# Optimization experiments

Hardware: AMD Instinct MI355X
Metric: run time of the kernel (lower is better)

## Reference

```python
import jax, jax.numpy as jnp
import numpy as np

HEADS = 4
DIM_HEAD = 32
DIM = 128
B, N, Hq, Wg = 2, 6, 32, 32   # batch, cameras, BEV grid
HK, WK = 28, 60               # image feature map


def _ln(x, g, b, eps=1e-5):
    mu = jnp.mean(x, axis=-1, keepdims=True)
    var = jnp.mean((x - mu) ** 2, axis=-1, keepdims=True)
    return (x - mu) * jax.lax.rsqrt(var + eps) * g + b


def setup_inputs() -> dict:
    key = jax.random.key(0)
    ks = jax.random.split(key, 12)
    s = 0.05  # weight scale to keep softmax logits well-conditioned
    inp = {
        'q': jax.random.normal(ks[0], (B, N, DIM, Hq, Wg), jnp.float32),
        'k': jax.random.normal(ks[1], (B, N, DIM, HK, WK), jnp.float32),
        'v': jax.random.normal(ks[2], (B, N, DIM, HK, WK), jnp.float32),
        'skip': jax.random.normal(ks[3], (B, DIM, Hq, Wg), jnp.float32),
        'q_ln_g': jnp.ones((DIM,), jnp.float32),
        'q_ln_b': jnp.zeros((DIM,), jnp.float32),
        'Wq': s * jax.random.normal(ks[4], (DIM, HEADS * DIM_HEAD), jnp.float32),
        'bq': jnp.zeros((HEADS * DIM_HEAD,), jnp.float32),
        'k_ln_g': jnp.ones((DIM,), jnp.float32),
        'k_ln_b': jnp.zeros((DIM,), jnp.float32),
        'Wk': s * jax.random.normal(ks[5], (DIM, HEADS * DIM_HEAD), jnp.float32),
        'bk': jnp.zeros((HEADS * DIM_HEAD,), jnp.float32),
        'v_ln_g': jnp.ones((DIM,), jnp.float32),
        'v_ln_b': jnp.zeros((DIM,), jnp.float32),
        'Wv': s * jax.random.normal(ks[6], (DIM, HEADS * DIM_HEAD), jnp.float32),
        'bv': jnp.zeros((HEADS * DIM_HEAD,), jnp.float32),
        'Wp': s * jax.random.normal(ks[7], (HEADS * DIM_HEAD, DIM), jnp.float32),
        'bp': jnp.zeros((DIM,), jnp.float32),
        'pre_g': jnp.ones((DIM,), jnp.float32),
        'pre_b': jnp.zeros((DIM,), jnp.float32),
        'W1': s * jax.random.normal(ks[8], (DIM, 2 * DIM), jnp.float32),
        'b1': jnp.zeros((2 * DIM,), jnp.float32),
        'W2': s * jax.random.normal(ks[9], (2 * DIM, DIM), jnp.float32),
        'b2': jnp.zeros((DIM,), jnp.float32),
        'post_g': jnp.ones((DIM,), jnp.float32),
        'post_b': jnp.zeros((DIM,), jnp.float32),
    }
    return inp


def reference(q, k, v, skip, q_ln_g, q_ln_b, Wq, bq, k_ln_g, k_ln_b, Wk, bk,
              v_ln_g, v_ln_b, Wv, bv, Wp, bp, pre_g, pre_b,
              W1, b1, W2, b2, post_g, post_b):
    b, n, d, H, W = q.shape
    Q = H * W
    K = k.shape[3] * k.shape[4]
    m, dh = HEADS, DIM_HEAD
    # b n d H W -> b n Q d   /  b n d h w -> b n K d  /  b (n K) d
    qf = q.transpose(0, 1, 3, 4, 2).reshape(b, n, Q, d)
    kf = k.transpose(0, 1, 3, 4, 2).reshape(b, n, K, d)
    vf = v.transpose(0, 1, 3, 4, 2).reshape(b, n * K, d)
    # norm -> linear, then split heads: b ... (m dh) -> (b m) ... dh
    qh = (_ln(qf, q_ln_g, q_ln_b) @ Wq + bq).reshape(b, n, Q, m, dh)
    qh = qh.transpose(0, 3, 1, 2, 4).reshape(b * m, n, Q, dh)
    kh = (_ln(kf, k_ln_g, k_ln_b) @ Wk + bk).reshape(b, n, K, m, dh)
    kh = kh.transpose(0, 3, 1, 2, 4).reshape(b * m, n, K, dh)
    vh = (_ln(vf, v_ln_g, v_ln_b) @ Wv + bv).reshape(b, n * K, m, dh)
    vh = vh.transpose(0, 2, 1, 3).reshape(b * m, n * K, dh)
    scale = dh ** -0.5
    dot = scale * jnp.einsum('anqd,ankd->anqk', qh, kh)   # (b m) n Q K
    dot = dot.transpose(0, 2, 1, 3).reshape(b * m, Q, n * K)  # fold views into keys
    att = jax.nn.softmax(dot, axis=-1)
    a = jnp.einsum('aqk,akd->aqd', att, vh)               # (b m) Q dh
    a = a.reshape(b, m, Q, dh).transpose(0, 2, 1, 3).reshape(b, Q, m * dh)
    z = a @ Wp + bp
    z = z + skip.transpose(0, 2, 3, 1).reshape(b, Q, d)
    z = _ln(z, pre_g, pre_b)
    z = z + (jax.nn.gelu(z @ W1 + b1, approximate=False) @ W2 + b2)
    z = _ln(z, post_g, post_b)
    return z.reshape(b, H, W, d).transpose(0, 3, 1, 2)
```

## Files before the change

### kernel.cpp

```cpp
#include <hip/hip_runtime.h>
#include <math.h>

#define NCAM 6
#define BSZ 2
#define SQL 1024
#define SKL 1680
#define NHEAD 4
#define DHEAD 32
#define QSCALE 0.25503494f

typedef unsigned short ushort_t;
typedef unsigned int uint_t;
typedef __attribute__((ext_vector_type(8))) short short8;
typedef __attribute__((ext_vector_type(4))) float f32x4;

#define MFMA16 __builtin_amdgcn_mfma_f32_16x16x32_bf16

__device__ __forceinline__ ushort_t f2bf(float x) {
  uint_t u = __builtin_bit_cast(uint_t, x);
  u += 0x7FFFu + ((u >> 16) & 1u);
  return (ushort_t)(u >> 16);
}

__device__ __forceinline__ float fast_gelu(float x) {
  const float ax = fabsf(x) * 0.70710678118654752f;
  const float tt = __builtin_amdgcn_rcpf(fmaf(0.3275911f, ax, 1.f));
  float poly = fmaf(tt, 1.061405429f, -1.453152027f);
  poly = fmaf(tt, poly, 1.421413741f);
  poly = fmaf(tt, poly, -0.284496736f);
  poly = fmaf(tt, poly, 0.254829592f);
  poly *= tt;
  const float e = __builtin_amdgcn_exp2f(-ax * ax * 1.4426950408889634f);
  float er = fmaf(-poly, e, 1.f);
  er = copysignf(er, x);
  return 0.5f * x * (1.f + er);
}

__global__ __launch_bounds__(256) void prep_kernel(
    const float* __restrict__ Wq, const float* __restrict__ qg, const float* __restrict__ qb, const float* __restrict__ bq,
    const float* __restrict__ Wk, const float* __restrict__ kg, const float* __restrict__ kbb, const float* __restrict__ bk,
    const float* __restrict__ Wv, const float* __restrict__ vg, const float* __restrict__ vbb, const float* __restrict__ bv,
    const float* __restrict__ Wp,
    const float* __restrict__ W1, const float* __restrict__ pre_g, const float* __restrict__ pre_b, const float* __restrict__ b1,
    const float* __restrict__ W2,
    ushort_t* WqT, ushort_t* WkT, ushort_t* WvT, ushort_t* WpT, ushort_t* W1T, ushort_t* W2T,
    float* uq, float* bbq, float* uk, float* bbk, float* uv, float* bbv, float* b1p) {
  const int mb = blockIdx.x;
  const float *W, *g = nullptr, *bln = nullptr, *bias = nullptr;
  ushort_t* WT; float *u = nullptr, *bb = nullptr;
  int kin = 128, nout = 128, ob;
  if (mb < 4)       { W=Wq; g=qg; bln=qb;   bias=bq; WT=WqT; u=uq; bb=bbq; ob=mb*32; }
  else if (mb < 8)  { W=Wk; g=kg; bln=kbb;  bias=bk; WT=WkT; u=uk; bb=bbk; ob=(mb-4)*32; }
  else if (mb < 12) { W=Wv; g=vg; bln=vbb;  bias=bv; WT=WvT; u=uv; bb=bbv; ob=(mb-8)*32; }
  else if (mb < 16) { W=Wp; WT=WpT; ob=(mb-12)*32; }
  else if (mb < 24) { W=W1; g=pre_g; bln=pre_b; bias=b1; WT=W1T; bb=b1p; nout=256; ob=(mb-16)*32; }
  else              { W=W2; WT=W2T; kin=256; ob=(mb-24)*32; }
  const int t = threadIdx.x;
  const int oc = t & 31, ig = t >> 5;
  const int out = ob + oc;
  const int nper = kin >> 3;
  float su = 0.f, sb = 0.f;
  for (int j = 0; j < nper; ++j) {
    const int in = ig * nper + j;
    const float wv_ = W[(size_t)in * nout + out];
    const float wg = g ? g[in] * wv_ : wv_;
    WT[(size_t)out * kin + in] = f2bf(wg);
    su += wg;
    if (bln) sb += bln[in] * wv_;
  }
  __shared__ float sU[8][32], sB[8][32];
  sU[ig][oc] = su; sB[ig][oc] = sb;
  __syncthreads();
  if (t < 32) {
    float tu = 0.f, tb = 0.f;
#pragma unroll
    for (int i = 0; i < 8; ++i) { tu += sU[i][t]; tb += sB[i][t]; }
    if (u)  u[ob + t] = tu;
    if (bb) bb[ob + t] = tb + (bias ? bias[ob + t] : 0.f);
  }
}

__global__ __launch_bounds__(256) void proj_mfma(
    const float* __restrict__ xq, const float* __restrict__ xk, const float* __restrict__ xv,
    const ushort_t* __restrict__ WqT, const ushort_t* __restrict__ WkT, const ushort_t* __restrict__ WvT,
    const float* __restrict__ uq, const float* __restrict__ uk, const float* __restrict__ uv,
    const float* __restrict__ bbq, const float* __restrict__ bbk, const float* __restrict__ bbv,
    ushort_t* __restrict__ Qh, ushort_t* __restrict__ Kh, ushort_t* __restrict__ Vt) {
  int blk = blockIdx.x;
  const float* x; const ushort_t* WT; const float* u; const float* bb;
  ushort_t* out; int S, ntile, vmode; float oscale;
  if (blk < 192)      { x=xq; WT=WqT; u=uq; bb=bbq; out=Qh; S=SQL; ntile=16; vmode=0; oscale=QSCALE; }
  else if (blk < 516) { blk-=192; x=xk; WT=WkT; u=uk; bb=bbk; out=Kh; S=SKL; ntile=27; vmode=0; oscale=1.f; }
  else                { blk-=516; x=xv; WT=WvT; u=uv; bb=bbv; out=Vt; S=SKL; ntile=27; vmode=1; oscale=1.f; }
  const int bn = blk / ntile;
  const int pos0 = (blk - bn * ntile) * 64;
  int valid = S - pos0; if (valid > 64) valid = 64;

  const int t = threadIdx.x;
  __shared__ ushort_t sX[64 * 128];
  __shared__ float sS1[16][64], sS2[16][64];
  __shared__ float sMu[64], sRs[64];

  {
    const int posq = t & 15, chg = t >> 4;
    int lp4 = 4 * posq; if (lp4 >= valid) lp4 = valid - 4;
    const float* xb = x + ((size_t)bn * 128 + chg * 8) * S + pos0 + lp4;
    float v[8][4];
#pragma unroll
    for (int i = 0; i < 8; ++i) {
      const float4 f = *((const float4*)(xb + (size_t)i * S));
      v[i][0] = f.x; v[i][1] = f.y; v[i][2] = f.z; v[i][3] = f.w;
    }
#pragma unroll
    for (int j = 0; j < 4; ++j) {
      float s1 = 0.f, s2 = 0.f;
#pragma unroll
      for (int i = 0; i < 8; ++i) { s1 += v[i][j]; s2 += v[i][j] * v[i][j]; }
      sS1[chg][lp4 + j] = s1; sS2[chg][lp4 + j] = s2;
    }
#pragma unroll
    for (int j = 0; j < 4; ++j) {
      const int pos = lp4 + j;
      short8 pk;
#pragma unroll
      for (int i = 0; i < 8; ++i) pk[i] = (short)f2bf(v[i][j]);
      const int phys = chg ^ (pos & 7);
      *((short8*)&sX[pos * 128 + phys * 8]) = pk;
    }
  }
  __syncthreads();
  if (t < 64) {
    float a1 = 0.f, a2 = 0.f;
#pragma unroll
    for (int g = 0; g < 16; ++g) { a1 += sS1[g][t]; a2 += sS2[g][t]; }
    const float mu = a1 * (1.f / 128.f);
    sMu[t] = mu; sRs[t] = rsqrtf(a2 * (1.f / 128.f) - mu * mu + 1e-5f);
  }
  __syncthreads();

  const int w = t >> 6, l = t & 63, lq = l & 15, quad = l >> 4;
  short8 af[2][4];
#pragma unroll
  for (int ms = 0; ms < 2; ++ms)
#pragma unroll
    for (int kk = 0; kk < 4; ++kk)
      af[ms][kk] = *((const short8*)(WT + (size_t)(w * 32 + ms * 16 + lq) * 128 + quad * 8 + kk * 32));
  f32x4 acc[4][2];
#pragma unroll
  for (int ns = 0; ns < 4; ++ns)
#pragma unroll
    for (int ms = 0; ms < 2; ++ms) acc[ns][ms] = (f32x4){0.f, 0.f, 0.f, 0.f};
#pragma unroll
  for (int ns = 0; ns < 4; ++ns) {
    short8 bf[4];
#pragma unroll
    for (int kk = 0; kk < 4; ++kk) {
      const int phys = (quad + 4 * kk) ^ (lq & 7);
      bf[kk] = *((const short8*)&sX[(ns * 16 + lq) * 128 + phys * 8]);
    }
#pragma unroll
    for (int ms = 0; ms < 2; ++ms) {
      f32x4 a = acc[ns][ms];
#pragma unroll
      for (int kk = 0; kk < 4; ++kk) a = MFMA16(af[ms][kk], bf[kk], a, 0, 0, 0);
      acc[ns][ms] = a;
    }
  }

  const int b_ = bn / NCAM, cam = bn - b_ * NCAM;
  const size_t slab = (size_t)((b_ * NHEAD + w) * NCAM + cam);
#pragma unroll
  for (int ms = 0; ms < 2; ++ms) {
    float uu[4], bv_[4];
#pragma unroll
    for (int r = 0; r < 4; ++r) {
      const int og = w * 32 + ms * 16 + quad * 4 + r;
      uu[r] = u[og]; bv_[r] = bb[og];
    }
#pragma unroll
    for (int ns = 0; ns < 4; ++ns) {
      const int p = ns * 16 + lq;
      if (p < valid) {
        const float mu = sMu[p], rs = sRs[p];
        float val[4];
#pragma unroll
        for (int r = 0; r < 4; ++r)
          val[r] = ((acc[ns][ms][r] - mu * uu[r]) * rs + bv_[r]) * oscale;
        if (vmode == 0) {
          ushort_t e0 = f2bf(val[0]), e1 = f2bf(val[1]), e2 = f2bf(val[2]), e3 = f2bf(val[3]);
          ushort_t* orow = out + (slab * S + pos0 + p) * 32 + ms * 16 + quad * 4;
          *((uint_t*)orow) = (uint_t)e0 | ((uint_t)e1 << 16);
          *((uint_t*)(orow + 2)) = (uint_t)e2 | ((uint_t)e3 << 16);
        } else {
#pragma unroll
          for (int r = 0; r < 4; ++r)
            out[(slab * 32 + ms * 16 + quad * 4 + r) * (size_t)SKL + pos0 + p] = f2bf(val[r]);
        }
      }
    }
  }
}

__global__ __launch_bounds__(512, 2) void attn_mfma(
    const ushort_t* __restrict__ Qh, const ushort_t* __restrict__ Kh,
    const ushort_t* __restrict__ Vt, ushort_t* __restrict__ Ab) {
  const int t = threadIdx.x;
  const int w = t >> 6, l = t & 63;
  const int lq = l & 15, quad = l >> 4;
  const int bm = blockIdx.x & 7;
  const int q0 = (blockIdx.x >> 3) * 32;
  const int camg = w >> 2, kq = w & 3;
  const int kstart = kq * 448;
  const int nfull = (kq == 3) ? 5 : 7;

  __shared__ ushort_t sP[8][2][16][72];
  __shared__ float sO[8][2][16][36];
  __shared__ float sL[8][2][16];

  f32x4 oA0 = {0.f,0.f,0.f,0.f}, oA1 = {0.f,0.f,0.f,0.f};
  f32x4 oB0 = {0.f,0.f,0.f,0.f}, oB1 = {0.f,0.f,0.f,0.f};
  float lA = 0.f, lB = 0.f;

  for (int nc = 0; nc < 3; ++nc) {
    const int n = camg * 3 + nc;
    const ushort_t* Kb = Kh + (size_t)(bm * NCAM + n) * SKL * 32;
    const ushort_t* Vb = Vt + (size_t)(bm * NCAM + n) * 32 * SKL;
    const ushort_t* Qbase = Qh + ((size_t)(bm * NCAM + n) * SQL + q0) * 32;
    const short8 qfA = *((const short8*)(Qbase + (size_t)lq * 32 + quad * 8));
    const short8 qfB = *((const short8*)(Qbase + (size_t)(16 + lq) * 32 + quad * 8));

    for (int kt = 0; kt < nfull; ++kt) {
      const int kb = kstart + kt * 64;
      short8 kf[4];
#pragma unroll
      for (int st = 0; st < 4; ++st)
        kf[st] = *((const short8*)(Kb + (size_t)(kb + st * 16 + lq) * 32 + quad * 8));
      const short8 v00 = *((const short8*)(Vb + (size_t)lq * SKL + kb + quad * 8));
      const short8 v01 = *((const short8*)(Vb + (size_t)lq * SKL + kb + 32 + quad * 8));
      const short8 v10 = *((const short8*)(Vb + (size_t)(16 + lq) * SKL + kb + quad * 8));
      const short8 v11 = *((const short8*)(Vb + (size_t)(16 + lq) * SKL + kb + 32 + quad * 8));

      f32x4 sA[4], sB[4];
#pragma unroll
      for (int st = 0; st < 4; ++st) {
        f32x4 z = {0.f, 0.f, 0.f, 0.f};
        sA[st] = MFMA16(kf[st], qfA, z, 0, 0, 0);
        sB[st] = MFMA16(kf[st], qfB, z, 0, 0, 0);
      }
      float lsA = 0.f, lsB = 0.f;
#pragma unroll
      for (int st = 0; st < 4; ++st) {
        const float a0 = __builtin_amdgcn_exp2f(sA[st][0]);
        const float a1 = __builtin_amdgcn_exp2f(sA[st][1]);
        const float a2 = __builtin_amdgcn_exp2f(sA[st][2]);
        const float a3 = __builtin_amdgcn_exp2f(sA[st][3]);
        const float b0 = __builtin_amdgcn_exp2f(sB[st][0]);
        const float b1 = __builtin_amdgcn_exp2f(sB[st][1]);
        const float b2 = __builtin_amdgcn_exp2f(sB[st][2]);
        const float b3 = __builtin_amdgcn_exp2f(sB[st][3]);
        lsA += (a0 + a1) + (a2 + a3);
        lsB += (b0 + b1) + (b2 + b3);
        const uint_t pa0 = __builtin_amdgcn_perm(__builtin_bit_cast(uint_t, a1), __builtin_bit_cast(uint_t, a0), 0x07060302u);
        const uint_t pa1 = __builtin_amdgcn_perm(__builtin_bit_cast(uint_t, a3), __builtin_bit_cast(uint_t, a2), 0x07060302u);
        const uint_t pb0 = __builtin_amdgcn_perm(__builtin_bit_cast(uint_t, b1), __builtin_bit_cast(uint_t, b0), 0x07060302u);
        const uint_t pb1 = __builtin_amdgcn_perm(__builtin_bit_cast(uint_t, b3), __builtin_bit_cast(uint_t, b2), 0x07060302u);
        *((uint2*)&sP[w][0][lq][st * 16 + quad * 4]) = make_uint2(pa0, pa1);
        *((uint2*)&sP[w][1][lq][st * 16 + quad * 4]) = make_uint2(pb0, pb1);
      }
      const short8 pfA0 = *((const short8*)&sP[w][0][lq][quad * 8]);
      const short8 pfA1 = *((const short8*)&sP[w][0][lq][32 + quad * 8]);
      const short8 pfB0 = *((const short8*)&sP[w][1][lq][quad * 8]);
      const short8 pfB1 = *((const short8*)&sP[w][1][lq][32 + quad * 8]);
      oA0 = MFMA16(v00, pfA0, oA0, 0, 0, 0);
      oA1 = MFMA16(v10, pfA0, oA1, 0, 0, 0);
      oB0 = MFMA16(v00, pfB0, oB0, 0, 0, 0);
      oB1 = MFMA16(v10, pfB0, oB1, 0, 0, 0);
      oA0 = MFMA16(v01, pfA1, oA0, 0, 0, 0);
      oA1 = MFMA16(v11, pfA1, oA1, 0, 0, 0);
      oB0 = MFMA16(v01, pfB1, oB0, 0, 0, 0);
      oB1 = MFMA16(v11, pfB1, oB1, 0, 0, 0);
      lsA += __shfl_xor(lsA, 16, 64);
      lsA += __shfl_xor(lsA, 32, 64);
      lsB += __shfl_xor(lsB, 16, 64);
      lsB += __shfl_xor(lsB, 32, 64);
      lA += lsA; lB += lsB;
    }

    if (kq == 3) {
      const int kb = kstart + 320;
      const short8 kf = *((const short8*)(Kb + (size_t)(kb + lq) * 32 + quad * 8));
      const short8 v00 = *((const short8*)(Vb + (size_t)lq * SKL + kb + quad * 8));
      const short8 v10 = *((const short8*)(Vb + (size_t)(16 + lq) * SKL + kb + quad * 8));
      f32x4 z = {0.f, 0.f, 0.f, 0.f};
      const f32x4 s0A = MFMA16(kf, qfA, z, 0, 0, 0);
      const f32x4 s0B = MFMA16(kf, qfB, z, 0, 0, 0);
      const float a0 = __builtin_amdgcn_exp2f(s0A[0]);
      const float a1 = __builtin_amdgcn_exp2f(s0A[1]);
      const float a2 = __builtin_amdgcn_exp2f(s0A[2]);
      const float a3 = __builtin_amdgcn_exp2f(s0A[3]);
      const float b0 = __builtin_amdgcn_exp2f(s0B[0]);
      const float b1 = __builtin_amdgcn_exp2f(s0B[1]);
      const float b2 = __builtin_amdgcn_exp2f(s0B[2]);
      const float b3 = __builtin_amdgcn_exp2f(s0B[3]);
      float lsA = (a0 + a1) + (a2 + a3);
      float lsB = (b0 + b1) + (b2 + b3);
      const uint_t pa0 = __builtin_amdgcn_perm(__builtin_bit_cast(uint_t, a1), __builtin_bit_cast(uint_t, a0), 0x07060302u);
      const uint_t pa1 = __builtin_amdgcn_perm(__builtin_bit_cast(uint_t, a3), __builtin_bit_cast(uint_t, a2), 0x07060302u);
      const uint_t pb0 = __builtin_amdgcn_perm(__builtin_bit_cast(uint_t, b1), __builtin_bit_cast(uint_t, b0), 0x07060302u);
      const uint_t pb1 = __builtin_amdgcn_perm(__builtin_bit_cast(uint_t, b3), __builtin_bit_cast(uint_t, b2), 0x07060302u);
      *((uint2*)&sP[w][0][lq][quad * 4]) = make_uint2(pa0, pa1);
      *((uint2*)&sP[w][0][lq][16 + quad * 4]) = make_uint2(0u, 0u);
      *((uint2*)&sP[w][1][lq][quad * 4]) = make_uint2(pb0, pb1);
      *((uint2*)&sP[w][1][lq][16 + quad * 4]) = make_uint2(0u, 0u);
      const short8 pfA0 = *((const short8*)&sP[w][0][lq][quad * 8]);
      const short8 pfB0 = *((const short8*)&sP[w][1][lq][quad * 8]);
      oA0 = MFMA16(v00, pfA0, oA0, 0, 0, 0);
      oA1 = MFMA16(v10, pfA0, oA1, 0, 0, 0);
      oB0 = MFMA16(v00, pfB0, oB0, 0, 0, 0);
      oB1 = MFMA16(v10, pfB0, oB1, 0, 0, 0);
      lsA += __shfl_xor(lsA, 16, 64);
      lsA += __shfl_xor(lsA, 32, 64);
      lsB += __shfl_xor(lsB, 16, 64);
      lsB += __shfl_xor(lsB, 32, 64);
      lA += lsA; lB += lsB;
    }
  }

  *((f32x4*)&sO[w][0][lq][quad * 4]) = oA0;
  *((f32x4*)&sO[w][0][lq][16 + quad * 4]) = oA1;
  *((f32x4*)&sO[w][1][lq][quad * 4]) = oB0;
  *((f32x4*)&sO[w][1][lq][16 + quad * 4]) = oB1;
  if (l < 16) { sL[w][0][l] = lA; sL[w][1][l] = lB; }
  __syncthreads();
  if (w < 2) {
    const int frag = w;
    float lf = 0.f;
    f32x4 a0 = {0.f, 0.f, 0.f, 0.f}, a1 = {0.f, 0.f, 0.f, 0.f};
#pragma unroll
    for (int ww = 0; ww < 8; ++ww) {
      lf += sL[ww][frag][lq];
      a0 += *((const f32x4*)&sO[ww][frag][lq][quad * 4]);
      a1 += *((const f32x4*)&sO[ww][frag][lq][16 + quad * 4]);
    }
    const float inv = 1.f / lf;
    const int b = bm >> 2, hm = bm & 3;
    ushort_t* op = Ab + ((size_t)b * SQL + q0 + frag * 16 + lq) * 128 + hm * 32 + quad * 4;
    ushort4 w0 = make_ushort4(f2bf(a0[0] * inv), f2bf(a0[1] * inv), f2bf(a0[2] * inv), f2bf(a0[3] * inv));
    ushort4 w1 = make_ushort4(f2bf(a1[0] * inv), f2bf(a1[1] * inv), f2bf(a1[2] * inv), f2bf(a1[3] * inv));
    *((ushort4*)op) = w0;
    *((ushort4*)(op + 16)) = w1;
  }
}

__global__ __launch_bounds__(256) void post_mfma(
    const ushort_t* __restrict__ Ab, const float* __restrict__ skip,
    const ushort_t* __restrict__ WpT, const float* __restrict__ bp,
    const float* __restrict__ pre_g, const float* __restrict__ pre_b,
    const ushort_t* __restrict__ W1T, const float* __restrict__ b1p,
    const ushort_t* __restrict__ W2T, const float* __restrict__ b2,
    const float* __restrict__ post_g, const float* __restrict__ post_b,
    float* __restrict__ out) {
  const int t = threadIdx.x;
  const int w = t >> 6, l = t & 63, lq = l & 15, quad = l >> 4;
  const int b = blockIdx.x >> 6;
  const int p0 = (blockIdx.x & 63) * 16;

  __shared__ float zf[16 * 132];
  __shared__ float sRes[16 * 132];
  __shared__ ushort_t sZb[16 * 128];
  __shared__ ushort_t sH[16 * 256];
  __shared__ float sMu[16], sRs[16];

  f32x4 z[2] = {{0.f,0.f,0.f,0.f},{0.f,0.f,0.f,0.f}};
#pragma unroll
  for (int kk = 0; kk < 4; ++kk) {
    const short8 bfr = *((const short8*)(Ab + ((size_t)b * SQL + p0 + lq) * 128 + quad * 8 + kk * 32));
#pragma unroll
    for (int ms = 0; ms < 2; ++ms) {
      const short8 afr = *((const short8*)(WpT + (size_t)(w * 32 + ms * 16 + lq) * 128 + quad * 8 + kk * 32));
      z[ms] = MFMA16(afr, bfr, z[ms], 0, 0, 0);
    }
  }
#pragma unroll
  for (int ms = 0; ms < 2; ++ms)
#pragma unroll
    for (int r = 0; r < 4; ++r) {
      const int o = w * 32 + ms * 16 + quad * 4 + r;
      zf[lq * 132 + o] = z[ms][r] + bp[o] + skip[(size_t)b * 131072 + (size_t)o * 1024 + p0 + lq];
    }
  __syncthreads();
  if (w == 0) {
    const int pos = l & 15, qr = l >> 4;
    float s1 = 0.f, s2 = 0.f;
#pragma unroll
    for (int j = 0; j < 32; ++j) { const float vv = zf[pos * 132 + qr * 32 + j]; s1 += vv; s2 += vv * vv; }
    s1 += __shfl_xor(s1, 16, 64); s1 += __shfl_xor(s1, 32, 64);
    s2 += __shfl_xor(s2, 16, 64); s2 += __shfl_xor(s2, 32, 64);
    const float mu = s1 * (1.f / 128.f);
    if (qr == 0) { sMu[pos] = mu; sRs[pos] = rsqrtf(s2 * (1.f / 128.f) - mu * mu + 1e-5f); }
  }
  __syncthreads();
  {
    const int pos = t & 15, grp = t >> 4;
    const float mu = sMu[pos], rs = sRs[pos];
    short8 pk;
#pragma unroll
    for (int i = 0; i < 8; ++i) {
      const int ch = grp * 8 + i;
      const float nv = (zf[pos * 132 + ch] - mu) * rs;
      pk[i] = (short)f2bf(nv);
      sRes[pos * 132 + ch] = nv * pre_g[ch] + pre_b[ch];
    }
    *((short8*)&sZb[pos * 128 + (grp ^ (pos & 7)) * 8]) = pk;
  }
  __syncthreads();
  f32x4 h[4];
#pragma unroll
  for (int ms = 0; ms < 4; ++ms) h[ms] = (f32x4){0.f, 0.f, 0.f, 0.f};
  short8 bz[4];
#pragma unroll
  for (int kk = 0; kk < 4; ++kk)
    bz[kk] = *((const short8*)&sZb[lq * 128 + ((quad + 4 * kk) ^ (lq & 7)) * 8]);
#pragma unroll
  for (int ms = 0; ms < 4; ++ms)
#pragma unroll
    for (int kk = 0; kk < 4; ++kk) {
      const short8 afr = *((const short8*)(W1T + (size_t)(w * 64 + ms * 16 + lq) * 128 + quad * 8 + kk * 32));
      h[ms] = MFMA16(afr, bz[kk], h[ms], 0, 0, 0);
    }
#pragma unroll
  for (int ms = 0; ms < 4; ++ms)
#pragma unroll
    for (int r = 0; r < 4; ++r) {
      const int o = w * 64 + ms * 16 + quad * 4 + r;
      const float hv = fast_gelu(h[ms][r] + b1p[o]);
      const int phys = (o >> 3) ^ (lq & 7);
      sH[lq * 256 + phys * 8 + (o & 7)] = f2bf(hv);
    }
  __syncthreads();
  f32x4 z2[2] = {{0.f,0.f,0.f,0.f},{0.f,0.f,0.f,0.f}};
#pragma unroll
  for (int kk = 0; kk < 8; ++kk) {
    const short8 bh = *((const short8*)&sH[lq * 256 + ((quad + 4 * kk) ^ (lq & 7)) * 8]);
#pragma unroll
    for (int ms = 0; ms < 2; ++ms) {
      const short8 afr = *((const short8*)(W2T + (size_t)(w * 32 + ms * 16 + lq) * 256 + quad * 8 + kk * 32));
      z2[ms] = MFMA16(afr, bh, z2[ms], 0, 0, 0);
    }
  }
  __syncthreads();
#pragma unroll
  for (int ms = 0; ms < 2; ++ms)
#pragma unroll
    for (int r = 0; r < 4; ++r) {
      const int o = w * 32 + ms * 16 + quad * 4 + r;
      zf[lq * 132 + o] = z2[ms][r] + b2[o] + sRes[lq * 132 + o];
    }
  __syncthreads();
  if (w == 0) {
    const int pos = l & 15, qr = l >> 4;
    float s1 = 0.f, s2 = 0.f;
#pragma unroll
    for (int j = 0; j < 32; ++j) { const float vv = zf[pos * 132 + qr * 32 + j]; s1 += vv; s2 += vv * vv; }
    s1 += __shfl_xor(s1, 16, 64); s1 += __shfl_xor(s1, 32, 64);
    s2 += __shfl_xor(s2, 16, 64); s2 += __shfl_xor(s2, 32, 64);
    const float mu = s1 * (1.f / 128.f);
    if (qr == 0) { sMu[pos] = mu; sRs[pos] = rsqrtf(s2 * (1.f / 128.f) + 1e-5f - mu * mu + mu * mu - mu * mu); }
  }
  __syncthreads();
  {
    const int pos = t & 15, grp = t >> 4;
    const float mu = sMu[pos], rs = sRs[pos];
#pragma unroll
    for (int i = 0; i < 8; ++i) {
      const int ch = grp * 8 + i;
      out[(size_t)b * 131072 + (size_t)ch * 1024 + p0 + pos] =
          (zf[pos * 132 + ch] - mu) * rs * post_g[ch] + post_b[ch];
    }
  }
}

extern "C" void kernel_launch(void* const* d_in, const int* in_sizes, int n_in,
                              void* d_out, int out_size, void* d_ws, size_t ws_size,
                              hipStream_t stream) {
  const float* q_in   = (const float*)d_in[0];
  const float* k_in   = (const float*)d_in[1];
  const float* v_in   = (const float*)d_in[2];
  const float* skip   = (const float*)d_in[3];
  const float* q_ln_g = (const float*)d_in[4];
  const float* q_ln_b = (const float*)d_in[5];
  const float* Wq     = (const float*)d_in[6];
  const float* bq     = (const float*)d_in[7];
  const float* k_ln_g = (const float*)d_in[8];
  const float* k_ln_b = (const float*)d_in[9];
  const float* Wk     = (const float*)d_in[10];
  const float* bk     = (const float*)d_in[11];
  const float* v_ln_g = (const float*)d_in[12];
  const float* v_ln_b = (const float*)d_in[13];
  const float* Wv     = (const float*)d_in[14];
  const float* bv     = (const float*)d_in[15];
  const float* Wp     = (const float*)d_in[16];
  const float* bp     = (const float*)d_in[17];
  const float* pre_g  = (const float*)d_in[18];
  const float* pre_b  = (const float*)d_in[19];
  const float* W1     = (const float*)d_in[20];
  const float* b1     = (const float*)d_in[21];
  const float* W2     = (const float*)d_in[22];
  const float* b2     = (const float*)d_in[23];
  const float* post_g = (const float*)d_in[24];
  const float* post_b = (const float*)d_in[25];

  char* base = (char*)d_ws;
  ushort_t* WqT = (ushort_t*)base; base += 16384 * 2;
  ushort_t* WkT = (ushort_t*)base; base += 16384 * 2;
  ushort_t* WvT = (ushort_t*)base; base += 16384 * 2;
  ushort_t* WpT = (ushort_t*)base; base += 16384 * 2;
  ushort_t* W1T = (ushort_t*)base; base += 32768 * 2;
  ushort_t* W2T = (ushort_t*)base; base += 32768 * 2;
  float* uq  = (float*)base; base += 128 * 4;
  float* bbq = (float*)base; base += 128 * 4;
  float* uk  = (float*)base; base += 128 * 4;
  float* bbk = (float*)base; base += 128 * 4;
  float* uv  = (float*)base; base += 128 * 4;
  float* bbv = (float*)base; base += 128 * 4;
  float* b1p = (float*)base; base += 256 * 4;
  base = (char*)(((size_t)base + 255) & ~(size_t)255);
  ushort_t* Qh = (ushort_t*)base; base += (size_t)1572864 * 2;
  ushort_t* Kh = (ushort_t*)base; base += (size_t)(2580480 + 4096) * 2;
  ushort_t* Vt = (ushort_t*)base; base += (size_t)(2580480 + 4096) * 2;
  ushort_t* Ab = (ushort_t*)base; base += (size_t)262144 * 2;
  float* out = (float*)d_out;

  prep_kernel<<<28, 256, 0, stream>>>(
      Wq, q_ln_g, q_ln_b, bq, Wk, k_ln_g, k_ln_b, bk, Wv, v_ln_g, v_ln_b, bv,
      Wp, W1, pre_g, pre_b, b1, W2,
      WqT, WkT, WvT, WpT, W1T, W2T, uq, bbq, uk, bbk, uv, bbv, b1p);
  proj_mfma<<<840, 256, 0, stream>>>(
      q_in, k_in, v_in, WqT, WkT, WvT, uq, uk, uv, bbq, bbk, bbv, Qh, Kh, Vt);
  attn_mfma<<<256, 512, 0, stream>>>(Qh, Kh, Vt, Ab);
  post_mfma<<<128, 256, 0, stream>>>(
      Ab, skip, WpT, bp, pre_g, pre_b, W1T, b1p, W2T, b2, post_g, post_b, out);
}
```

Before: 174.2 us.

## Double-buffer attention P tiles, fully unroll loops, and halve post-kernel block size

The attention kernel now double-buffers the per-wave P staging in shared memory, fully unrolls the camera and key-tile loops through lambdas, and splits the quarter-3 wave path so the compiler can interleave tiles. Launch bounds drop to one block per SM to allow more registers. The post kernel processes 8 positions per block (16 rows computed, half clamped and discarded) with twice as many blocks for more parallelism, at the cost of duplicated MFMA work. The variance expression is also cleaned up.

```diff
diff --git a/kernel.cpp b/kernel.cpp
--- a/kernel.cpp
+++ b/kernel.cpp
@@ -201,7 +201,7 @@
   }
 }
 
-__global__ __launch_bounds__(512, 2) void attn_mfma(
+__global__ __launch_bounds__(512, 1) void attn_mfma(
     const ushort_t* __restrict__ Qh, const ushort_t* __restrict__ Kh,
     const ushort_t* __restrict__ Vt, ushort_t* __restrict__ Ab) {
   const int t = threadIdx.x;
@@ -211,9 +211,8 @@
   const int q0 = (blockIdx.x >> 3) * 32;
   const int camg = w >> 2, kq = w & 3;
   const int kstart = kq * 448;
-  const int nfull = (kq == 3) ? 5 : 7;
-
-  __shared__ ushort_t sP[8][2][16][72];
+
+  __shared__ ushort_t sP[8][2][2][16][72];
   __shared__ float sO[8][2][16][36];
   __shared__ float sL[8][2][16];
 
@@ -221,108 +220,128 @@
   f32x4 oB0 = {0.f,0.f,0.f,0.f}, oB1 = {0.f,0.f,0.f,0.f};
   float lA = 0.f, lB = 0.f;
 
-  for (int nc = 0; nc < 3; ++nc) {
-    const int n = camg * 3 + nc;
-    const ushort_t* Kb = Kh + (size_t)(bm * NCAM + n) * SKL * 32;
-    const ushort_t* Vb = Vt + (size_t)(bm * NCAM + n) * 32 * SKL;
-    const ushort_t* Qbase = Qh + ((size_t)(bm * NCAM + n) * SQL + q0) * 32;
-    const short8 qfA = *((const short8*)(Qbase + (size_t)lq * 32 + quad * 8));
-    const short8 qfB = *((const short8*)(Qbase + (size_t)(16 + lq) * 32 + quad * 8));
-
-    for (int kt = 0; kt < nfull; ++kt) {
-      const int kb = kstart + kt * 64;
-      short8 kf[4];
-#pragma unroll
-      for (int st = 0; st < 4; ++st)
-        kf[st] = *((const short8*)(Kb + (size_t)(kb + st * 16 + lq) * 32 + quad * 8));
-      const short8 v00 = *((const short8*)(Vb + (size_t)lq * SKL + kb + quad * 8));
-      const short8 v01 = *((const short8*)(Vb + (size_t)lq * SKL + kb + 32 + quad * 8));
-      const short8 v10 = *((const short8*)(Vb + (size_t)(16 + lq) * SKL + kb + quad * 8));
-      const short8 v11 = *((const short8*)(Vb + (size_t)(16 + lq) * SKL + kb + 32 + quad * 8));
-
-      f32x4 sA[4], sB[4];
-#pragma unroll
-      for (int st = 0; st < 4; ++st) {
-        f32x4 z = {0.f, 0.f, 0.f, 0.f};
-        sA[st] = MFMA16(kf[st], qfA, z, 0, 0, 0);
-        sB[st] = MFMA16(kf[st], qfB, z, 0, 0, 0);
-      }
-      float lsA = 0.f, lsB = 0.f;
-#pragma unroll
-      for (int st = 0; st < 4; ++st) {
-        const float a0 = __builtin_amdgcn_exp2f(sA[st][0]);
-        const float a1 = __builtin_amdgcn_exp2f(sA[st][1]);
-        const float a2 = __builtin_amdgcn_exp2f(sA[st][2]);
-        const float a3 = __builtin_amdgcn_exp2f(sA[st][3]);
-        const float b0 = __builtin_amdgcn_exp2f(sB[st][0]);
-        const float b1 = __builtin_amdgcn_exp2f(sB[st][1]);
-        const float b2 = __builtin_amdgcn_exp2f(sB[st][2]);
-        const float b3 = __builtin_amdgcn_exp2f(sB[st][3]);
-        lsA += (a0 + a1) + (a2 + a3);
-        lsB += (b0 + b1) + (b2 + b3);
-        const uint_t pa0 = __builtin_amdgcn_perm(__builtin_bit_cast(uint_t, a1), __builtin_bit_cast(uint_t, a0), 0x07060302u);
-        const uint_t pa1 = __builtin_amdgcn_perm(__builtin_bit_cast(uint_t, a3), __builtin_bit_cast(uint_t, a2), 0x07060302u);
-        const uint_t pb0 = __builtin_amdgcn_perm(__builtin_bit_cast(uint_t, b1), __builtin_bit_cast(uint_t, b0), 0x07060302u);
-        const uint_t pb1 = __builtin_amdgcn_perm(__builtin_bit_cast(uint_t, b3), __builtin_bit_cast(uint_t, b2), 0x07060302u);
-        *((uint2*)&sP[w][0][lq][st * 16 + quad * 4]) = make_uint2(pa0, pa1);
-        *((uint2*)&sP[w][1][lq][st * 16 + quad * 4]) = make_uint2(pb0, pb1);
-      }
-      const short8 pfA0 = *((const short8*)&sP[w][0][lq][quad * 8]);
-      const short8 pfA1 = *((const short8*)&sP[w][0][lq][32 + quad * 8]);
-      const short8 pfB0 = *((const short8*)&sP[w][1][lq][quad * 8]);
-      const short8 pfB1 = *((const short8*)&sP[w][1][lq][32 + quad * 8]);
-      oA0 = MFMA16(v00, pfA0, oA0, 0, 0, 0);
-      oA1 = MFMA16(v10, pfA0, oA1, 0, 0, 0);
-      oB0 = MFMA16(v00, pfB0, oB0, 0, 0, 0);
-      oB1 = MFMA16(v10, pfB0, oB1, 0, 0, 0);
-      oA0 = MFMA16(v01, pfA1, oA0, 0, 0, 0);
-      oA1 = MFMA16(v11, pfA1, oA1, 0, 0, 0);
-      oB0 = MFMA16(v01, pfB1, oB0, 0, 0, 0);
-      oB1 = MFMA16(v11, pfB1, oB1, 0, 0, 0);
-      lsA += __shfl_xor(lsA, 16, 64);
-      lsA += __shfl_xor(lsA, 32, 64);
-      lsB += __shfl_xor(lsB, 16, 64);
-      lsB += __shfl_xor(lsB, 32, 64);
-      lA += lsA; lB += lsB;
-    }
-
-    if (kq == 3) {
-      const int kb = kstart + 320;
-      const short8 kf = *((const short8*)(Kb + (size_t)(kb + lq) * 32 + quad * 8));
-      const short8 v00 = *((const short8*)(Vb + (size_t)lq * SKL + kb + quad * 8));
-      const short8 v10 = *((const short8*)(Vb + (size_t)(16 + lq) * SKL + kb + quad * 8));
+  auto tile_full = [&](const ushort_t* Kb, const ushort_t* Vb, int kb, int buf,
+                       short8 qfA, short8 qfB) {
+    short8 kf[4];
+#pragma unroll
+    for (int st = 0; st < 4; ++st)
+      kf[st] = *((const short8*)(Kb + (size_t)(kb + st * 16 + lq) * 32 + quad * 8));
+    const short8 v00 = *((const short8*)(Vb + (size_t)lq * SKL + kb + quad * 8));
+    const short8 v01 = *((const short8*)(Vb + (size_t)lq * SKL + kb + 32 + quad * 8));
+    const short8 v10 = *((const short8*)(Vb + (size_t)(16 + lq) * SKL + kb + quad * 8));
+    const short8 v11 = *((const short8*)(Vb + (size_t)(16 + lq) * SKL + kb + 32 + quad * 8));
+
+    f32x4 sA[4], sB[4];
+#pragma unroll
+    for (int st = 0; st < 4; ++st) {
       f32x4 z = {0.f, 0.f, 0.f, 0.f};
-      const f32x4 s0A = MFMA16(kf, qfA, z, 0, 0, 0);
-      const f32x4 s0B = MFMA16(kf, qfB, z, 0, 0, 0);
-      const float a0 = __builtin_amdgcn_exp2f(s0A[0]);
-      const float a1 = __builtin_amdgcn_exp2f(s0A[1]);
-      const float a2 = __builtin_amdgcn_exp2f(s0A[2]);
-      const float a3 = __builtin_amdgcn_exp2f(s0A[3]);
-      const float b0 = __builtin_amdgcn_exp2f(s0B[0]);
-      const float b1 = __builtin_amdgcn_exp2f(s0B[1]);
-      const float b2 = __builtin_amdgcn_exp2f(s0B[2]);
-      const float b3 = __builtin_amdgcn_exp2f(s0B[3]);
-      float lsA = (a0 + a1) + (a2 + a3);
-      float lsB = (b0 + b1) + (b2 + b3);
+      sA[st] = MFMA16(kf[st], qfA, z, 0, 0, 0);
+      sB[st] = MFMA16(kf[st], qfB, z, 0, 0, 0);
+    }
+    float lsA = 0.f, lsB = 0.f;
+#pragma unroll
+    for (int st = 0; st < 4; ++st) {
+      const float a0 = __builtin_amdgcn_exp2f(sA[st][0]);
+      const float a1 = __builtin_amdgcn_exp2f(sA[st][1]);
+      const float a2 = __builtin_amdgcn_exp2f(sA[st][2]);
+      const float a3 = __builtin_amdgcn_exp2f(sA[st][3]);
+      const float b0 = __builtin_amdgcn_exp2f(sB[st][0]);
+      const float b1 = __builtin_amdgcn_exp2f(sB[st][1]);
+      const float b2 = __builtin_amdgcn_exp2f(sB[st][2]);
+      const float b3 = __builtin_amdgcn_exp2f(sB[st][3]);
+      lsA += (a0 + a1) + (a2 + a3);
+      lsB += (b0 + b1) + (b2 + b3);
       const uint_t pa0 = __builtin_amdgcn_perm(__builtin_bit_cast(uint_t, a1), __builtin_bit_cast(uint_t, a0), 0x07060302u);
       const uint_t pa1 = __builtin_amdgcn_perm(__builtin_bit_cast(uint_t, a3), __builtin_bit_cast(uint_t, a2), 0x07060302u);
       const uint_t pb0 = __builtin_amdgcn_perm(__builtin_bit_cast(uint_t, b1), __builtin_bit_cast(uint_t, b0), 0x07060302u);
       const uint_t pb1 = __builtin_amdgcn_perm(__builtin_bit_cast(uint_t, b3), __builtin_bit_cast(uint_t, b2), 0x07060302u);
-      *((uint2*)&sP[w][0][lq][quad * 4]) = make_uint2(pa0, pa1);
-      *((uint2*)&sP[w][0][lq][16 + quad * 4]) = make_uint2(0u, 0u);
-      *((uint2*)&sP[w][1][lq][quad * 4]) = make_uint2(pb0, pb1);
-      *((uint2*)&sP[w][1][lq][16 + quad * 4]) = make_uint2(0u, 0u);
-      const short8 pfA0 = *((const short8*)&sP[w][0][lq][quad * 8]);
-      const short8 pfB0 = *((const short8*)&sP[w][1][lq][quad * 8]);
-      oA0 = MFMA16(v00, pfA0, oA0, 0, 0, 0);
-      oA1 = MFMA16(v10, pfA0, oA1, 0, 0, 0);
-      oB0 = MFMA16(v00, pfB0, oB0, 0, 0, 0);
-      oB1 = MFMA16(v10, pfB0, oB1, 0, 0, 0);
-      lsA += __shfl_xor(lsA, 16, 64);
-      lsA += __shfl_xor(lsA, 32, 64);
-      lsB += __shfl_xor(lsB, 16, 64);
-      lsB += __shfl_xor(lsB, 32, 64);
-      lA += lsA; lB += lsB;
+      *((uint2*)&sP[w][buf][0][lq][st * 16 + quad * 4]) = make_uint2(pa0, pa1);
+      *((uint2*)&sP[w][buf][1][lq][st * 16 + quad * 4]) = make_uint2(pb0, pb1);
+    }
+    const short8 pfA0 = *((const short8*)&sP[w][buf][0][lq][quad * 8]);
+    const short8 pfA1 = *((const short8*)&sP[w][buf][0][lq][32 + quad * 8]);
+    const short8 pfB0 = *((const short8*)&sP[w][buf][1][lq][quad * 8]);
+    const short8 pfB1 = *((const short8*)&sP[w][buf][1][lq][32 + quad * 8]);
+    oA0 = MFMA16(v00, pfA0, oA0, 0, 0, 0);
+    oA1 = MFMA16(v10, pfA0, oA1, 0, 0, 0);
+    oB0 = MFMA16(v00, pfB0, oB0, 0, 0, 0);
+    oB1 = MFMA16(v10, pfB0, oB1, 0, 0, 0);
+    oA0 = MFMA16(v01, pfA1, oA0, 0, 0, 0);
+    oA1 = MFMA16(v11, pfA1, oA1, 0, 0, 0);
+    oB0 = MFMA16(v01, pfB1, oB0, 0, 0, 0);
+    oB1 = MFMA16(v11, pfB1, oB1, 0, 0, 0);
+    lsA += __shfl_xor(lsA, 16, 64);
+    lsA += __shfl_xor(lsA, 32, 64);
+    lsB += __shfl_xor(lsB, 16, 64);
+    lsB += __shfl_xor(lsB, 32, 64);
+    lA += lsA; lB += lsB;
+  };
+
+  auto tile_tail = [&](const ushort_t* Kb, const ushort_t* Vb, int kb, int buf,
+                       short8 qfA, short8 qfB) {
+    const short8 kf = *((const short8*)(Kb + (size_t)(kb + lq) * 32 + quad * 8));
+    const short8 v00 = *((const short8*)(Vb + (size_t)lq * SKL + kb + quad * 8));
+    const short8 v10 = *((const short8*)(Vb + (size_t)(16 + lq) * SKL + kb + quad * 8));
+    f32x4 z = {0.f, 0.f, 0.f, 0.f};
+    const f32x4 s0A = MFMA16(kf, qfA, z, 0, 0, 0);
+    const f32x4 s0B = MFMA16(kf, qfB, z, 0, 0, 0);
+    const float a0 = __builtin_amdgcn_exp2f(s0A[0]);
+    const float a1 = __builtin_amdgcn_exp2f(s0A[1]);
+    const float a2 = __builtin_amdgcn_exp2f(s0A[2]);
+    const float a3 = __builtin_amdgcn_exp2f(s0A[3]);
+    const float b0 = __builtin_amdgcn_exp2f(s0B[0]);
+    const float b1 = __builtin_amdgcn_exp2f(s0B[1]);
+    const float b2 = __builtin_amdgcn_exp2f(s0B[2]);
+    const float b3 = __builtin_amdgcn_exp2f(s0B[3]);
+    float lsA = (a0 + a1) + (a2 + a3);
+    float lsB = (b0 + b1) + (b2 + b3);
+    const uint_t pa0 = __builtin_amdgcn_perm(__builtin_bit_cast(uint_t, a1), __builtin_bit_cast(uint_t, a0), 0x07060302u);
+    const uint_t pa1 = __builtin_amdgcn_perm(__builtin_bit_cast(uint_t, a3), __builtin_bit_cast(uint_t, a2), 0x07060302u);
+    const uint_t pb0 = __builtin_amdgcn_perm(__builtin_bit_cast(uint_t, b1), __builtin_bit_cast(uint_t, b0), 0x07060302u);
+    const uint_t pb1 = __builtin_amdgcn_perm(__builtin_bit_cast(uint_t, b3), __builtin_bit_cast(uint_t, b2), 0x07060302u);
+    *((uint2*)&sP[w][buf][0][lq][quad * 4]) = make_uint2(pa0, pa1);
+    *((uint2*)&sP[w][buf][0][lq][16 + quad * 4]) = make_uint2(0u, 0u);
+    *((uint2*)&sP[w][buf][1][lq][quad * 4]) = make_uint2(pb0, pb1);
+    *((uint2*)&sP[w][buf][1][lq][16 + quad * 4]) = make_uint2(0u, 0u);
+    const short8 pfA0 = *((const short8*)&sP[w][buf][0][lq][quad * 8]);
+    const short8 pfB0 = *((const short8*)&sP[w][buf][1][lq][quad * 8]);
+    oA0 = MFMA16(v00, pfA0, oA0, 0, 0, 0);
+    oA1 = MFMA16(v10, pfA0, oA1, 0, 0, 0);
+    oB0 = MFMA16(v00, pfB0, oB0, 0, 0, 0);
+    oB1 = MFMA16(v10, pfB0, oB1, 0, 0, 0);
+    lsA += __shfl_xor(lsA, 16, 64);
+    lsA += __shfl_xor(lsA, 32, 64);
+    lsB += __shfl_xor(lsB, 16, 64);
+    lsB += __shfl_xor(lsB, 32, 64);
+    lA += lsA; lB += lsB;
+  };
+
+  if (kq < 3) {
+#pragma unroll
+    for (int nc = 0; nc < 3; ++nc) {
+      const int n = camg * 3 + nc;
+      const ushort_t* Kb = Kh + (size_t)(bm * NCAM + n) * SKL * 32;
+      const ushort_t* Vb = Vt + (size_t)(bm * NCAM + n) * 32 * SKL;
+      const ushort_t* Qb = Qh + ((size_t)(bm * NCAM + n) * SQL + q0) * 32;
+      const short8 qfA = *((const short8*)(Qb + (size_t)lq * 32 + quad * 8));
+      const short8 qfB = *((const short8*)(Qb + (size_t)(16 + lq) * 32 + quad * 8));
+#pragma unroll
+      for (int kt = 0; kt < 7; ++kt)
+        tile_full(Kb, Vb, kstart + kt * 64, (nc * 7 + kt) & 1, qfA, qfB);
+    }
+  } else {
+#pragma unroll
+    for (int nc = 0; nc < 3; ++nc) {
+      const int n = camg * 3 + nc;
+      const ushort_t* Kb = Kh + (size_t)(bm * NCAM + n) * SKL * 32;
+      const ushort_t* Vb = Vt + (size_t)(bm * NCAM + n) * 32 * SKL;
+      const ushort_t* Qb = Qh + ((size_t)(bm * NCAM + n) * SQL + q0) * 32;
+      const short8 qfA = *((const short8*)(Qb + (size_t)lq * 32 + quad * 8));
+      const short8 qfB = *((const short8*)(Qb + (size_t)(16 + lq) * 32 + quad * 8));
+#pragma unroll
+      for (int kt = 0; kt < 5; ++kt)
+        tile_full(Kb, Vb, kstart + kt * 64, kt & 1, qfA, qfB);
+      tile_tail(Kb, Vb, kstart + 320, 1, qfA, qfB);
     }
   }
 
@@ -362,8 +381,9 @@
     float* __restrict__ out) {
   const int t = threadIdx.x;
   const int w = t >> 6, l = t & 63, lq = l & 15, quad = l >> 4;
-  const int b = blockIdx.x >> 6;
-  const int p0 = (blockIdx.x & 63) * 16;
+  const int b = blockIdx.x >> 7;
+  const int p0 = (blockIdx.x & 127) * 8;
+  const int rp = (p0 + lq < SQL) ? (p0 + lq) : (SQL - 1);
 
   __shared__ float zf[16 * 132];
   __shared__ float sRes[16 * 132];
@@ -374,7 +394,7 @@
   f32x4 z[2] = {{0.f,0.f,0.f,0.f},{0.f,0.f,0.f,0.f}};
 #pragma unroll
   for (int kk = 0; kk < 4; ++kk) {
-    const short8 bfr = *((const short8*)(Ab + ((size_t)b * SQL + p0 + lq) * 128 + quad * 8 + kk * 32));
+    const short8 bfr = *((const short8*)(Ab + ((size_t)b * SQL + rp) * 128 + quad * 8 + kk * 32));
 #pragma unroll
     for (int ms = 0; ms < 2; ++ms) {
       const short8 afr = *((const short8*)(WpT + (size_t)(w * 32 + ms * 16 + lq) * 128 + quad * 8 + kk * 32));
@@ -386,7 +406,8 @@
 #pragma unroll
     for (int r = 0; r < 4; ++r) {
       const int o = w * 32 + ms * 16 + quad * 4 + r;
-      zf[lq * 132 + o] = z[ms][r] + bp[o] + skip[(size_t)b * 131072 + (size_t)o * 1024 + p0 + lq];
+      const int rr = (p0 + lq < SQL) ? (p0 + lq) : (SQL - 1);
+      zf[lq * 132 + o] = z[ms][r] + bp[o] + skip[(size_t)b * 131072 + (size_t)o * 1024 + rr];
     }
   __syncthreads();
   if (w == 0) {
@@ -465,17 +486,19 @@
     s1 += __shfl_xor(s1, 16, 64); s1 += __shfl_xor(s1, 32, 64);
     s2 += __shfl_xor(s2, 16, 64); s2 += __shfl_xor(s2, 32, 64);
     const float mu = s1 * (1.f / 128.f);
-    if (qr == 0) { sMu[pos] = mu; sRs[pos] = rsqrtf(s2 * (1.f / 128.f) + 1e-5f - mu * mu + mu * mu - mu * mu); }
+    if (qr == 0) { sMu[pos] = mu; sRs[pos] = rsqrtf(s2 * (1.f / 128.f) - mu * mu + 1e-5f); }
   }
   __syncthreads();
   {
     const int pos = t & 15, grp = t >> 4;
-    const float mu = sMu[pos], rs = sRs[pos];
-#pragma unroll
-    for (int i = 0; i < 8; ++i) {
-      const int ch = grp * 8 + i;
-      out[(size_t)b * 131072 + (size_t)ch * 1024 + p0 + pos] =
-          (zf[pos * 132 + ch] - mu) * rs * post_g[ch] + post_b[ch];
+    if (pos < 8) {
+      const float mu = sMu[pos], rs = sRs[pos];
+#pragma unroll
+      for (int i = 0; i < 8; ++i) {
+        const int ch = grp * 8 + i;
+        out[(size_t)b * 131072 + (size_t)ch * 1024 + p0 + pos] =
+            (zf[pos * 132 + ch] - mu) * rs * post_g[ch] + post_b[ch];
+      }
     }
   }
 }
@@ -538,6 +561,6 @@
   proj_mfma<<<840, 256, 0, stream>>>(
       q_in, k_in, v_in, WqT, WkT, WvT, uq, uk, uv, bbq, bbk, bbv, Qh, Kh, Vt);
   attn_mfma<<<256, 512, 0, stream>>>(Qh, Kh, Vt, Ab);
-  post_mfma<<<128, 256, 0, stream>>>(
+  post_mfma<<<256, 256, 0, stream>>>(
       Ab, skip, WpT, bp, pre_g, pre_b, W1T, b1p, W2T, b2, post_g, post_b, out);
 }
```

After: 195.6 us. 1.12x slower.
